# Optimization experiments

Hardware: AMD Instinct MI355X
Metric: run time of the kernel (lower is better)

Reference implementation:

```python
import jax, jax.numpy as jnp
import numpy as np

N_NODES = 10000
N_EDGES = 320000
MUL0, MUL1 = 64, 32        # input irreps: 64x0e + 32x1e
EDGE_DIM = 64
W_NUMEL = 224              # 64+64+32+32+32 per-edge uvu path weights
DENOM = 32.0
SQRT3 = 3.0 ** 0.5
INV_SQRT3 = 1.0 / SQRT3
INV_SQRT2 = 2.0 ** -0.5


def setup_inputs() -> dict:
    key = jax.random.key(0)
    ks = jax.random.split(key, 12)

    def lin(k, fi, fo):
        return (jax.random.normal(k, (fi, fo), jnp.float32) / np.float32(np.sqrt(fi)))

    return {
        "node_feature": jax.random.normal(ks[0], (N_NODES, MUL0 + 3 * MUL1), jnp.float32),
        "edge_attr": jax.random.normal(ks[1], (N_EDGES, 3), jnp.float32),
        "edge_feature": jax.random.normal(ks[2], (N_EDGES, EDGE_DIM), jnp.float32),
        "W_skip0": lin(ks[3], MUL0, 96),
        "W_skip1": lin(ks[4], MUL1, 32),
        "W_nl0": lin(ks[5], MUL0, MUL0),
        "W_nl1": lin(ks[6], MUL1, MUL1),
        "W_fc1": lin(ks[7], EDGE_DIM, 64),
        "W_fc2": lin(ks[8], 64, W_NUMEL),
        "W_out_s": lin(ks[9], 96, 96),
        "W_out_v": lin(ks[10], 128, 32),
        "edge_index": jax.random.randint(ks[11], (2, N_EDGES), 0, N_NODES),
    }


def _forward(node_feature, edge_attr, edge_feature, W_skip0, W_skip1, W_nl0, W_nl1,
             W_fc1, W_fc2, W_out_s, W_out_v, edge_index):
    N = node_feature.shape[0]
    E = edge_attr.shape[0]
    s = node_feature[:, :MUL0]                       # [N,64] l=0 scalars
    v = node_feature[:, MUL0:].reshape(N, MUL1, 3)   # [N,32,3] l=1 vectors

    # skip_linear: in_irreps -> gate irreps (96x0e + 32x1e); per-l mixing of multiplicities
    skip_s = s @ W_skip0
    skip_v = jnp.einsum('nmi,mk->nki', v, W_skip1)

    # node_linear: in_irreps -> in_irreps
    s = s @ W_nl0
    v = jnp.einsum('nmi,mk->nki', v, W_nl1)

    # spherical harmonics (normalize=True, 'component'): Y0 = 1, Y1 = sqrt(3) * r_hat
    rhat = edge_attr / jnp.linalg.norm(edge_attr, axis=-1, keepdims=True)
    sh1 = SQRT3 * rhat                               # [E,3]

    # edge-conditioned TP weights: FC net (relu MLP, no bias)
    w = jax.nn.relu(edge_feature @ W_fc1) @ W_fc2    # [E,224]
    w0, w1, w2, w3, w4 = jnp.split(w, [64, 128, 160, 192], axis=-1)

    src, dst = edge_index[0], edge_index[1]
    xs = s[dst]                                      # gather: [E,64]
    xv = v[dst]                                      # gather: [E,32,3]

    # uvu CG paths (sh0 component == 1)
    out0a = w0 * xs                                                         # 0e x 0e -> 0e
    out0b = w3 * (jnp.einsum('emi,ei->em', xv, sh1) * INV_SQRT3)            # 1e x 1e -> 0e
    out1a = (w1 * xs)[:, :, None] * sh1[:, None, :]                         # 0e x 1e -> 1e
    out1b = w2[:, :, None] * xv                                             # 1e x 0e -> 1e
    out1c = w4[:, :, None] * (jnp.cross(xv, sh1[:, None, :]) * INV_SQRT2)   # 1e x 1e -> 1e

    # sorted irreps_mid layout: [96 scalars | 128 vectors * 3] = 480
    tp = jnp.concatenate([out0a, out0b,
                          out1a.reshape(E, -1), out1b.reshape(E, -1), out1c.reshape(E, -1)],
                         axis=-1)                    # [E,480]

    # scatter-sum to destination nodes, then divide by denominator
    agg = jax.ops.segment_sum(tp, src, num_segments=N) / DENOM

    # dropout(p=0.0) on l=0 channels -> identity
    agg_s = agg[:, :96]
    agg_v = agg[:, 96:].reshape(N, 128, 3)

    # node_linear_2: tp_irreps_out -> gate irreps, plus skip connection
    out_s = agg_s @ W_out_s + skip_s
    out_v = jnp.einsum('nmi,mk->nki', agg_v, W_out_v) + skip_v

    # equivariant gate: 64 scalars (silu) | 32 gate scalars (sigmoid) * 32 vectors
    fs = jax.nn.silu(out_s[:, :MUL0])
    gate = jax.nn.sigmoid(out_s[:, MUL0:MUL0 + 32])
    gv = gate[:, :, None] * out_v
    return jnp.concatenate([fs, gv.reshape(N, -1)], axis=-1)  # [N,160]


def reference(node_feature, edge_attr, edge_feature, W_skip0, W_skip1, W_nl0, W_nl1,
              W_fc1, W_fc2, W_out_s, W_out_v, edge_index):
    return _forward(node_feature, edge_attr, edge_feature, W_skip0, W_skip1, W_nl0, W_nl1,
                    W_fc1, W_fc2, W_out_s, W_out_v, edge_index)
```

## Files before the change

kernel.cpp:

```cpp
#include <hip/hip_runtime.h>
#include <math.h>

#define N_NODES 10000
#define N_EDGES 320000
#define TILES 8
#define NBLK (N_EDGES / (32 * TILES))

#define SQRT3F     1.7320508075688772f
#define INV_SQRT3F 0.5773502691896258f
#define INV_SQRT2F 0.7071067811865476f

typedef short bf16x8 __attribute__((ext_vector_type(8)));
typedef short b16x4  __attribute__((ext_vector_type(4)));
typedef float f32x4  __attribute__((ext_vector_type(4)));
typedef unsigned int u32;

static __device__ __forceinline__ unsigned short f2b(float f) {
    unsigned int u = __float_as_uint(f);
    unsigned int r = (u + 0x7fffu + ((u >> 16) & 1u)) >> 16;
    return (unsigned short)r;
}
static __device__ __forceinline__ float b2f(unsigned short h) {
    return __uint_as_float(((unsigned int)h) << 16);
}

static __device__ __forceinline__ void gl_lds16(const void* g, void* l) {
    __builtin_amdgcn_global_load_lds(
        (const __attribute__((address_space(1))) u32*)g,
        (__attribute__((address_space(3))) u32*)l,
        16, 0, 0);
}

__global__ __launch_bounds__(256) void prep_kernel(
    const float* __restrict__ nf,
    const float* __restrict__ Wnl0,
    const float* __restrict__ Wnl1,
    const float* __restrict__ Wfc1,
    const float* __restrict__ Wfc2,
    const float* __restrict__ Wout_s,
    const float* __restrict__ Wout_v,
    const float* __restrict__ Wskip0,
    const float* __restrict__ Wskip1,
    const int* __restrict__ eidx,
    float* __restrict__ st_vt32,
    unsigned short* __restrict__ st_vt16,
    unsigned short* __restrict__ W1T,
    unsigned short* __restrict__ W2T,
    unsigned short* __restrict__ WsCombT,
    unsigned short* __restrict__ WvCombT,
    int* __restrict__ cnt)
{
    const int b = blockIdx.x;
    const int tid = threadIdx.x;
    if (b < 6250) {
        int gid = b * 256 + tid;
        if (gid >= N_NODES * 160) return;
        int n = gid / 160;
        int j = gid - n * 160;
        const float* nfn = nf + (size_t)n * 160;
        float acc = 0.f;
        if (j < 64) {
            #pragma unroll 8
            for (int k = 0; k < 64; ++k) acc += nfn[k] * Wnl0[k * 64 + j];
        } else {
            int t = j - 64;
            int i = t >> 5, k = t & 31;
            #pragma unroll 8
            for (int m = 0; m < 32; ++m) acc += nfn[64 + m * 3 + i] * Wnl1[m * 32 + k];
        }
        st_vt32[(size_t)n * 160 + j] = acc;
        st_vt16[(size_t)n * 160 + j] = f2b(acc);
    } else if (b < 7500) {
        int e = (b - 6250) * 256 + tid;
        if (e < N_EDGES) atomicAdd(&cnt[eidx[e]], 1);
    } else if (b < 7572) {
        int idx = (b - 7500) * 256 + tid;
        if (idx < 4096) {
            int n = idx >> 6, k = idx & 63;
            W1T[idx] = f2b(Wfc1[k * 64 + n]);
        } else if (idx < 18432) {
            int j = idx - 4096;
            int n = j >> 6, k = j & 63;
            W2T[j] = f2b(Wfc2[k * 224 + n]);
        }
    } else {
        int idx = (b - 7572) * 256 + tid;
        if (idx < 15360) {
            int n = idx / 160, k = idx - n * 160;
            float v = (k < 96) ? Wout_s[k * 96 + n] : Wskip0[(k - 96) * 96 + n];
            WsCombT[idx] = f2b(v);
        } else if (idx < 20480) {
            int j = idx - 15360;
            int n = j / 160, k = j - n * 160;
            float v = (k < 128) ? Wout_v[k * 32 + n] : Wskip1[(k - 128) * 32 + n];
            WvCombT[j] = f2b(v);
        }
    }
}

__global__ __launch_bounds__(1024) void scan_kernel(
    const int* __restrict__ cnt, int* __restrict__ row_start)
{
    __shared__ int part[1024];
    const int t = threadIdx.x;
    const int CH = 10;
    int base = t * CH;
    int s = 0;
    for (int i = 0; i < CH; ++i) {
        int idx = base + i;
        if (idx < N_NODES) s += cnt[idx];
    }
    part[t] = s;
    __syncthreads();
    for (int off = 1; off < 1024; off <<= 1) {
        int v = (t >= off) ? part[t - off] : 0;
        __syncthreads();
        part[t] += v;
        __syncthreads();
    }
    int run = (t == 0) ? 0 : part[t - 1];
    for (int i = 0; i < CH; ++i) {
        int idx = base + i;
        if (idx < N_NODES) { row_start[idx] = run; run += cnt[idx]; }
    }
    if (t == 1023) row_start[N_NODES] = run;
}

__global__ __launch_bounds__(256) void scatter_kernel(
    const int* __restrict__ eidx, const float* __restrict__ edge_attr,
    const int* __restrict__ row_start,
    int* __restrict__ fill, int* __restrict__ order,
    int* __restrict__ src_srt, int* __restrict__ dst_srt,
    float* __restrict__ sh_srt)
{
    int e = blockIdx.x * 256 + threadIdx.x;
    if (e >= N_EDGES) return;
    int s = eidx[e];
    int p = atomicAdd(&fill[s], 1) + row_start[s];
    order[p] = e;
    src_srt[p] = s;
    dst_srt[p] = eidx[N_EDGES + e];
    float x = edge_attr[(size_t)e * 3 + 0];
    float y = edge_attr[(size_t)e * 3 + 1];
    float z = edge_attr[(size_t)e * 3 + 2];
    float inv = SQRT3F / sqrtf(x * x + y * y + z * z);
    sh_srt[(size_t)p * 4 + 0] = x * inv;
    sh_srt[(size_t)p * 4 + 1] = y * inv;
    sh_srt[(size_t)p * 4 + 2] = z * inv;
    sh_srt[(size_t)p * 4 + 3] = 0.f;
}

__global__ __launch_bounds__(256, 7) void edge_mlp(
    const unsigned short* __restrict__ W1T,
    const unsigned short* __restrict__ W2T,
    const int* __restrict__ order,
    const float* __restrict__ edge_feature,
    unsigned short* __restrict__ w_srt)
{
    __shared__ __align__(16) unsigned short A1[32 * 64];
    __shared__ __align__(16) unsigned short Hs[32 * 64];
    __shared__ __align__(16) unsigned short w_s[32 * 224];
    __shared__ int eid_s[32 * TILES];

    const int tid  = threadIdx.x;
    const int lane = tid & 63;
    const int wv   = tid >> 6;
    const int l15  = lane & 15;
    const int g    = lane >> 4;
    const int p0   = blockIdx.x * (32 * TILES);

    bf16x8 w1b0 = *reinterpret_cast<const bf16x8*>(&W1T[(wv * 16 + l15) * 64 + g * 8]);
    bf16x8 w1b1 = *reinterpret_cast<const bf16x8*>(&W1T[(wv * 16 + l15) * 64 + 32 + g * 8]);
    bf16x8 w2b0[4], w2b1[4];
    #pragma unroll
    for (int ii = 0; ii < 4; ++ii) {
        int nt = wv * 4 + ii;
        w2b0[ii] = *reinterpret_cast<const bf16x8*>(&W2T[(nt * 16 + l15) * 64 + g * 8]);
        w2b1[ii] = *reinterpret_cast<const bf16x8*>(&W2T[(nt * 16 + l15) * 64 + 32 + g * 8]);
    }

    if (tid < 32 * TILES) eid_s[tid] = order[p0 + tid];
    __syncthreads();

    f32x4 efr[2];
    auto load_ef = [&](int t) {
        int ebase = t * 32;
        #pragma unroll
        for (int r = 0; r < 2; ++r) {
            int q = tid + r * 256;
            int el = q >> 4, qf = q & 15;
            efr[r] = *reinterpret_cast<const f32x4*>(
                edge_feature + (size_t)eid_s[ebase + el] * 64 + qf * 4);
        }
    };
    auto write_ef = [&]() {
        #pragma unroll
        for (int r = 0; r < 2; ++r) {
            int q = tid + r * 256;
            int el = q >> 4, f0 = (q & 15) * 4;
            b16x4 h;
            #pragma unroll
            for (int j = 0; j < 4; ++j) h[j] = (short)f2b(efr[r][j]);
            *reinterpret_cast<b16x4*>(&A1[el * 64 + (f0 ^ ((el & 7) << 3))]) = h;
        }
    };

    load_ef(0);

    for (int t = 0; t < TILES; ++t) {
        write_ef();
        __syncthreads();
        if (t < TILES - 1) load_ef(t + 1);

        {
            const int nt = wv;
            #pragma unroll
            for (int mt = 0; mt < 2; ++mt) {
                f32x4 c4 = {0.f, 0.f, 0.f, 0.f};
                int ra = mt * 16 + l15;
                int sw = (ra & 7) << 3;
                bf16x8 a0 = *reinterpret_cast<const bf16x8*>(&A1[ra * 64 + ((g * 8) ^ sw)]);
                bf16x8 a1 = *reinterpret_cast<const bf16x8*>(&A1[ra * 64 + ((32 + g * 8) ^ sw)]);
                c4 = __builtin_amdgcn_mfma_f32_16x16x32_bf16(a0, w1b0, c4, 0, 0, 0);
                c4 = __builtin_amdgcn_mfma_f32_16x16x32_bf16(a1, w1b1, c4, 0, 0, 0);
                #pragma unroll
                for (int r = 0; r < 4; ++r) {
                    int row = mt * 16 + g * 4 + r;
                    int col = nt * 16 + l15;
                    Hs[row * 64 + (col ^ ((row & 7) << 3))] = f2b(fmaxf(c4[r], 0.f));
                }
            }
        }
        __syncthreads();

        {
            #pragma unroll
            for (int ii = 0; ii < 4; ++ii) {
                int nt = wv * 4 + ii;
                #pragma unroll
                for (int mt = 0; mt < 2; ++mt) {
                    f32x4 c4 = {0.f, 0.f, 0.f, 0.f};
                    int ra = mt * 16 + l15;
                    int sw = (ra & 7) << 3;
                    bf16x8 a0 = *reinterpret_cast<const bf16x8*>(&Hs[ra * 64 + ((g * 8) ^ sw)]);
                    bf16x8 a1 = *reinterpret_cast<const bf16x8*>(&Hs[ra * 64 + ((32 + g * 8) ^ sw)]);
                    c4 = __builtin_amdgcn_mfma_f32_16x16x32_bf16(a0, w2b0[ii], c4, 0, 0, 0);
                    c4 = __builtin_amdgcn_mfma_f32_16x16x32_bf16(a1, w2b1[ii], c4, 0, 0, 0);
                    if (nt < 14) {
                        #pragma unroll
                        for (int r = 0; r < 4; ++r) {
                            int row = mt * 16 + g * 4 + r;
                            w_s[row * 224 + nt * 16 + l15] = f2b(c4[r]);
                        }
                    }
                }
            }
        }
        __syncthreads();

        {
            const size_t gbase = (size_t)(p0 + t * 32) * 224;
            for (int idx = tid; idx < 896; idx += 256) {
                *reinterpret_cast<f32x4*>(&w_srt[gbase + idx * 8]) =
                    *reinterpret_cast<const f32x4*>(&w_s[idx * 8]);
            }
        }
    }
}

__global__ __launch_bounds__(256, 7) void node_msg(
    const int* __restrict__ row_start,
    const int* __restrict__ dst_srt,
    const float* __restrict__ sh_srt,
    const unsigned short* __restrict__ w_srt,
    const float* __restrict__ st_vt32,
    float* __restrict__ agg)
{
    __shared__ __align__(16) float df[32 * 160];
    __shared__ float aggbuf[480];
    __shared__ float sh_c[32][4];

    const int n   = (blockIdx.x & 7) * 1250 + (blockIdx.x >> 3);
    const int tid = threadIdx.x;
    const int p_start = row_start[n];
    const int p_end   = row_start[n + 1];

    const int tid2 = tid & 127;
    const int half = tid >> 7;
    int region, cb, iv;
    if (tid2 < 48)       { region = 0; cb = tid2 & 15;        iv = tid2 >> 4; }
    else if (tid2 < 64)  { region = 1; cb = tid2 - 48;        iv = 0; }
    else if (tid2 < 88)  { region = 2; cb = (tid2 - 64) & 7;  iv = (tid2 - 64) >> 3; }
    else if (tid2 < 112) { region = 3; cb = (tid2 - 88) & 7;  iv = (tid2 - 88) >> 3; }
    else if (tid2 < 120) { region = 4; cb = tid2 - 112;       iv = 0; }
    else                 { region = 5; cb = 0; iv = 0; }
    int rbase = 0, woff = 0, doff = 0;
    if (region == 0)      { rbase = 96 + iv * 64 + 4 * cb;  woff = 64 + 4 * cb;  doff = 4 * cb; }
    else if (region == 1) { rbase = 4 * cb;                 woff = 4 * cb;       doff = 4 * cb; }
    else if (region == 2) { rbase = 288 + iv * 32 + 4 * cb; woff = 128 + 4 * cb; doff = 64 + iv * 32 + 4 * cb; }
    else if (region == 3) { rbase = 384 + iv * 32 + 4 * cb; woff = 192 + 4 * cb; }
    else if (region == 4) { rbase = 64 + 4 * cb;            woff = 160 + 4 * cb; }
    int i1 = iv + 1; if (i1 == 3) i1 = 0;
    int i2 = 3 - iv - i1;

    f32x4 acc = {0.f, 0.f, 0.f, 0.f};

    for (int pb = p_start; pb < p_end; pb += 32) {
        const int nvalid = min(p_end - pb, 32);
        const int qlimit = nvalid * 40;
        __syncthreads();

        if (tid < nvalid) {
            *reinterpret_cast<f32x4*>(&sh_c[tid][0]) =
                *reinterpret_cast<const f32x4*>(&sh_srt[(size_t)(pb + tid) * 4]);
        }
        #pragma unroll
        for (int r = 0; r < 5; ++r) {
            int idx = tid + r * 256;
            if (idx < qlimit) {
                int el = idx / 40, off = idx - el * 40;
                int d = dst_srt[pb + el];
                gl_lds16(st_vt32 + (size_t)d * 160 + off * 4, &df[idx * 4]);
            }
        }
        __syncthreads();

        if (region < 5) {
            const int e0l = half * 16;
            #pragma unroll 4
            for (int j2 = 0; j2 < 16; ++j2) {
                int el = e0l + j2;
                if (el >= nvalid) break;
                const float* dfp = &df[el * 160];
                const unsigned short* we = w_srt + (size_t)(pb + el) * 224;
                b16x4 w = *reinterpret_cast<const b16x4*>(we + woff);
                if (region == 0) {
                    f32x4 x = *reinterpret_cast<const f32x4*>(dfp + doff);
                    float sh = sh_c[el][iv];
                    #pragma unroll
                    for (int j = 0; j < 4; ++j)
                        acc[j] += b2f((unsigned short)w[j]) * x[j] * sh;
                } else if (region == 1 || region == 2) {
                    f32x4 x = *reinterpret_cast<const f32x4*>(dfp + doff);
                    #pragma unroll
                    for (int j = 0; j < 4; ++j)
                        acc[j] += b2f((unsigned short)w[j]) * x[j];
                } else if (region == 3) {
                    f32x4 xA = *reinterpret_cast<const f32x4*>(dfp + 64 + i1 * 32 + 4 * cb);
                    f32x4 xB = *reinterpret_cast<const f32x4*>(dfp + 64 + i2 * 32 + 4 * cb);
                    float shA = sh_c[el][i1], shB = sh_c[el][i2];
                    #pragma unroll
                    for (int j = 0; j < 4; ++j)
                        acc[j] += b2f((unsigned short)w[j]) *
                                  (xA[j] * shB - xB[j] * shA) * INV_SQRT2F;
                } else {
                    f32x4 x0 = *reinterpret_cast<const f32x4*>(dfp + 64 + 4 * cb);
                    f32x4 x1 = *reinterpret_cast<const f32x4*>(dfp + 96 + 4 * cb);
                    f32x4 x2 = *reinterpret_cast<const f32x4*>(dfp + 128 + 4 * cb);
                    float s0 = sh_c[el][0], s1 = sh_c[el][1], s2 = sh_c[el][2];
                    #pragma unroll
                    for (int j = 0; j < 4; ++j)
                        acc[j] += b2f((unsigned short)w[j]) *
                                  (x0[j] * s0 + x1[j] * s1 + x2[j] * s2) * INV_SQRT3F;
                }
            }
        }
    }

    __syncthreads();
    if (half == 0 && region < 5) {
        #pragma unroll
        for (int j = 0; j < 4; ++j) aggbuf[rbase + j] = acc[j];
    }
    __syncthreads();
    if (half == 1 && region < 5) {
        #pragma unroll
        for (int j = 0; j < 4; ++j) aggbuf[rbase + j] += acc[j];
    }
    __syncthreads();
    if (tid < 120) {
        *reinterpret_cast<f32x4*>(&agg[(size_t)n * 480 + tid * 4]) =
            *reinterpret_cast<const f32x4*>(&aggbuf[tid * 4]);
    }
}

__global__ __launch_bounds__(256) void out_gemm(
    const float* __restrict__ agg,
    const float* __restrict__ nf,
    const unsigned short* __restrict__ WsCombT,
    const unsigned short* __restrict__ WvCombT,
    float* __restrict__ out)
{
    __shared__ float os_l[32][96];
    __shared__ float ov_l[3][32][32];

    const int n0  = blockIdx.x * 32;
    const int tid = threadIdx.x;
    const int lane = tid & 63;
    const int wv   = tid >> 6;
    const int l15  = lane & 15;
    const int g    = lane >> 4;

    #pragma unroll
    for (int jj = 0; jj < 6; ++jj) {
        int job = wv * 6 + jj;
        bool isS;
        int mt, nt, ii = 0;
        if (job < 12) { isS = true;  mt = job & 1; nt = job >> 1; }
        else { int j = job - 12; isS = false; ii = j >> 2; mt = (j >> 1) & 1; nt = j & 1; }

        int ra = mt * 16 + l15;
        int n  = min(n0 + ra, N_NODES - 1);
        const float* aggn = agg + (size_t)n * 480;
        const float* nfn  = nf + (size_t)n * 160;
        const unsigned short* WT = isS ? WsCombT : WvCombT;

        f32x4 c4 = {0.f, 0.f, 0.f, 0.f};
        #pragma unroll
        for (int kk = 0; kk < 5; ++kk) {
            int k0 = kk * 32 + g * 8;
            float av[8];
            if (isS) {
                if (k0 < 96) {
                    f32x4 p0 = *reinterpret_cast<const f32x4*>(aggn + k0);
                    f32x4 p1 = *reinterpret_cast<const f32x4*>(aggn + k0 + 4);
                    #pragma unroll
                    for (int j = 0; j < 4; ++j) { av[j] = p0[j] * (1.f/32.f); av[4+j] = p1[j] * (1.f/32.f); }
                } else {
                    f32x4 p0 = *reinterpret_cast<const f32x4*>(nfn + (k0 - 96));
                    f32x4 p1 = *reinterpret_cast<const f32x4*>(nfn + (k0 - 96) + 4);
                    #pragma unroll
                    for (int j = 0; j < 4; ++j) { av[j] = p0[j]; av[4+j] = p1[j]; }
                }
            } else {
                if (k0 < 128) {
                    int base = (k0 < 64) ? (96 + ii * 64 + k0)
                             : (k0 < 96) ? (288 + ii * 32 + (k0 - 64))
                                         : (384 + ii * 32 + (k0 - 96));
                    f32x4 p0 = *reinterpret_cast<const f32x4*>(aggn + base);
                    f32x4 p1 = *reinterpret_cast<const f32x4*>(aggn + base + 4);
                    #pragma unroll
                    for (int j = 0; j < 4; ++j) { av[j] = p0[j] * (1.f/32.f); av[4+j] = p1[j] * (1.f/32.f); }
                } else {
                    #pragma unroll
                    for (int j = 0; j < 8; ++j)
                        av[j] = nfn[64 + (k0 - 128 + j) * 3 + ii];
                }
            }
            bf16x8 a;
            #pragma unroll
            for (int j = 0; j < 8; ++j) a[j] = (short)f2b(av[j]);
            bf16x8 bfr = *reinterpret_cast<const bf16x8*>(
                WT + (size_t)(nt * 16 + l15) * 160 + k0);
            c4 = __builtin_amdgcn_mfma_f32_16x16x32_bf16(a, bfr, c4, 0, 0, 0);
        }
        #pragma unroll
        for (int r = 0; r < 4; ++r) {
            int row = mt * 16 + g * 4 + r;
            int col = nt * 16 + l15;
            if (isS) os_l[row][col] = c4[r];
            else     ov_l[ii][row][col] = c4[r];
        }
    }
    __syncthreads();

    for (int idx = tid; idx < 32 * 160; idx += 256) {
        int r = idx / 160, c = idx - r * 160;
        int n = n0 + r;
        if (n < N_NODES) {
            if (c < 64) {
                float x = os_l[r][c];
                out[(size_t)n * 160 + c] = x / (1.f + expf(-x));
            } else {
                int t = c - 64;
                int k = t / 3, i = t - 3 * k;
                float gg = os_l[r][64 + k];
                gg = 1.f / (1.f + expf(-gg));
                out[(size_t)n * 160 + c] = gg * ov_l[i][r][k];
            }
        }
    }
}

__global__ __launch_bounds__(256, 3) void edge_conv_fused(
    const unsigned short* __restrict__ W1T,
    const unsigned short* __restrict__ W2T,
    const int* __restrict__ order,
    const int* __restrict__ src_srt,
    const int* __restrict__ dst_srt,
    const float* __restrict__ sh_srt,
    const float* __restrict__ edge_feature,
    const unsigned short* __restrict__ st_vt16,
    float* __restrict__ agg)
{
    __shared__ __align__(16) unsigned short A1[32 * 64];
    __shared__ __align__(16) unsigned short Hs[32 * 64];
    __shared__ __align__(16) unsigned short w_s[32 * 224];
    __shared__ __align__(16) unsigned short df[2][32 * 160];
    __shared__ int   eid_s[32 * TILES];
    __shared__ int   src_s[32 * TILES];
    __shared__ int   dst_s[32 * TILES];
    __shared__ float sh_s[32 * TILES][4];

    const int tid  = threadIdx.x;
    const int lane = tid & 63;
    const int wv   = tid >> 6;
    const int l15  = lane & 15;
    const int g    = lane >> 4;
    const int p0   = blockIdx.x * (32 * TILES);

    bf16x8 w1b0 = *reinterpret_cast<const bf16x8*>(&W1T[(wv * 16 + l15) * 64 + g * 8]);
    bf16x8 w1b1 = *reinterpret_cast<const bf16x8*>(&W1T[(wv * 16 + l15) * 64 + 32 + g * 8]);
    bf16x8 w2b0[4], w2b1[4];
    #pragma unroll
    for (int ii = 0; ii < 4; ++ii) {
        int nt = wv * 4 + ii;
        w2b0[ii] = *reinterpret_cast<const bf16x8*>(&W2T[(nt * 16 + l15) * 64 + g * 8]);
        w2b1[ii] = *reinterpret_cast<const bf16x8*>(&W2T[(nt * 16 + l15) * 64 + 32 + g * 8]);
    }

    for (int b = tid; b < 32 * TILES; b += 256) {
        int p = p0 + b;
        eid_s[b] = order[p];
        src_s[b] = src_srt[p];
        dst_s[b] = dst_srt[p];
        *reinterpret_cast<f32x4*>(&sh_s[b][0]) =
            *reinterpret_cast<const f32x4*>(&sh_srt[(size_t)p * 4]);
    }
    __syncthreads();

    const int tid2 = tid & 127;
    int region, cb, iv;
    if (tid2 < 48)       { region = 0; cb = tid2 & 15;        iv = tid2 >> 4; }
    else if (tid2 < 64)  { region = 1; cb = tid2 - 48;        iv = 0; }
    else if (tid2 < 88)  { region = 2; cb = (tid2 - 64) & 7;  iv = (tid2 - 64) >> 3; }
    else if (tid2 < 112) { region = 3; cb = (tid2 - 88) & 7;  iv = (tid2 - 88) >> 3; }
    else if (tid2 < 120) { region = 4; cb = tid2 - 112;       iv = 0; }
    else                 { region = 5; cb = 0; iv = 0; }
    int rbase = 0, woff = 0, doff = 0;
    if (region == 0)      { rbase = 96 + iv * 64 + 4 * cb;  woff = 64 + 4 * cb;  doff = 4 * cb; }
    else if (region == 1) { rbase = 4 * cb;                 woff = 4 * cb;       doff = 4 * cb; }
    else if (region == 2) { rbase = 288 + iv * 32 + 4 * cb; woff = 128 + 4 * cb; doff = 64 + iv * 32 + 4 * cb; }
    else if (region == 3) { rbase = 384 + iv * 32 + 4 * cb; woff = 192 + 4 * cb; }
    else if (region == 4) { rbase = 64 + 4 * cb;            woff = 160 + 4 * cb; }
    int i1 = iv + 1; if (i1 == 3) i1 = 0;
    int i2 = 3 - iv - i1;

    f32x4 acc = {0.f, 0.f, 0.f, 0.f};
    int cur = src_s[(tid >> 7) * 16];

    f32x4 efr[2];
    auto load_ef = [&](int t) {
        int ebase = t * 32;
        #pragma unroll
        for (int r = 0; r < 2; ++r) {
            int q = tid + r * 256;
            int el = q >> 4, qf = q & 15;
            efr[r] = *reinterpret_cast<const f32x4*>(
                edge_feature + (size_t)eid_s[ebase + el] * 64 + qf * 4);
        }
    };
    auto write_ef = [&]() {
        #pragma unroll
        for (int r = 0; r < 2; ++r) {
            int q = tid + r * 256;
            int el = q >> 4, f0 = (q & 15) * 4;
            b16x4 h;
            #pragma unroll
            for (int j = 0; j < 4; ++j) h[j] = (short)f2b(efr[r][j]);
            *reinterpret_cast<b16x4*>(&A1[el * 64 + (f0 ^ ((el & 7) << 3))]) = h;
        }
    };
    auto issue_df = [&](int t, int b) {
        int ebase = t * 32;
        #pragma unroll
        for (int r = 0; r < 3; ++r) {
            int idx = tid + r * 256;
            if (idx < 640) {
                int el = idx / 20, off = idx - el * 20;
                gl_lds16(st_vt16 + (size_t)dst_s[ebase + el] * 160 + off * 8,
                         &df[b][idx * 8]);
            }
        }
    };

    issue_df(0, 0);
    load_ef(0);

    for (int t = 0; t < TILES; ++t) {
        const int b = t & 1;
        write_ef();
        __syncthreads();
        if (t < TILES - 1) {
            issue_df(t + 1, b ^ 1);
            load_ef(t + 1);
        }
        {
            const int nt = wv;
            #pragma unroll
            for (int mt = 0; mt < 2; ++mt) {
                f32x4 c4 = {0.f, 0.f, 0.f, 0.f};
                int ra = mt * 16 + l15;
                int sw = (ra & 7) << 3;
                bf16x8 a0 = *reinterpret_cast<const bf16x8*>(&A1[ra * 64 + ((g * 8) ^ sw)]);
                bf16x8 a1 = *reinterpret_cast<const bf16x8*>(&A1[ra * 64 + ((32 + g * 8) ^ sw)]);
                c4 = __builtin_amdgcn_mfma_f32_16x16x32_bf16(a0, w1b0, c4, 0, 0, 0);
                c4 = __builtin_amdgcn_mfma_f32_16x16x32_bf16(a1, w1b1, c4, 0, 0, 0);
                #pragma unroll
                for (int r = 0; r < 4; ++r) {
                    int row = mt * 16 + g * 4 + r;
                    int col = nt * 16 + l15;
                    Hs[row * 64 + (col ^ ((row & 7) << 3))] = f2b(fmaxf(c4[r], 0.f));
                }
            }
        }
        __syncthreads();
        {
            #pragma unroll
            for (int ii = 0; ii < 4; ++ii) {
                int nt = wv * 4 + ii;
                #pragma unroll
                for (int mt = 0; mt < 2; ++mt) {
                    f32x4 c4 = {0.f, 0.f, 0.f, 0.f};
                    int ra = mt * 16 + l15;
                    int sw = (ra & 7) << 3;
                    bf16x8 a0 = *reinterpret_cast<const bf16x8*>(&Hs[ra * 64 + ((g * 8) ^ sw)]);
                    bf16x8 a1 = *reinterpret_cast<const bf16x8*>(&Hs[ra * 64 + ((32 + g * 8) ^ sw)]);
                    c4 = __builtin_amdgcn_mfma_f32_16x16x32_bf16(a0, w2b0[ii], c4, 0, 0, 0);
                    c4 = __builtin_amdgcn_mfma_f32_16x16x32_bf16(a1, w2b1[ii], c4, 0, 0, 0);
                    if (nt < 14) {
                        #pragma unroll
                        for (int r = 0; r < 4; ++r) {
                            int row = mt * 16 + g * 4 + r;
                            w_s[row * 224 + nt * 16 + l15] = f2b(c4[r]);
                        }
                    }
                }
            }
        }
        __syncthreads();
        if (region < 5) {
            const int e0l = (tid >> 7) * 16;
            #pragma unroll 4
            for (int j2 = 0; j2 < 16; ++j2) {
                int el = e0l + j2;
                int eg = t * 32 + el;
                int s = src_s[eg];
                if (s != cur) {
                    #pragma unroll
                    for (int j = 0; j < 4; ++j)
                        atomicAdd(&agg[(size_t)cur * 480 + rbase + j], acc[j]);
                    acc = (f32x4){0.f, 0.f, 0.f, 0.f};
                    cur = s;
                }
                const unsigned short* dfp = &df[b][el * 160];
                const unsigned short* we  = &w_s[el * 224];
                b16x4 w = *reinterpret_cast<const b16x4*>(we + woff);
                if (region == 0) {
                    b16x4 x = *reinterpret_cast<const b16x4*>(dfp + doff);
                    float sh = sh_s[eg][iv];
                    #pragma unroll
                    for (int j = 0; j < 4; ++j)
                        acc[j] += b2f((unsigned short)w[j]) * b2f((unsigned short)x[j]) * sh;
                } else if (region == 1 || region == 2) {
                    b16x4 x = *reinterpret_cast<const b16x4*>(dfp + doff);
                    #pragma unroll
                    for (int j = 0; j < 4; ++j)
                        acc[j] += b2f((unsigned short)w[j]) * b2f((unsigned short)x[j]);
                } else if (region == 3) {
                    b16x4 xA = *reinterpret_cast<const b16x4*>(dfp + 64 + i1 * 32 + 4 * cb);
                    b16x4 xB = *reinterpret_cast<const b16x4*>(dfp + 64 + i2 * 32 + 4 * cb);
                    float shA = sh_s[eg][i1], shB = sh_s[eg][i2];
                    #pragma unroll
                    for (int j = 0; j < 4; ++j)
                        acc[j] += b2f((unsigned short)w[j]) *
                                  (b2f((unsigned short)xA[j]) * shB -
                                   b2f((unsigned short)xB[j]) * shA) * INV_SQRT2F;
                } else {
                    b16x4 x0 = *reinterpret_cast<const b16x4*>(dfp + 64 + 4 * cb);
                    b16x4 x1 = *reinterpret_cast<const b16x4*>(dfp + 96 + 4 * cb);
                    b16x4 x2 = *reinterpret_cast<const b16x4*>(dfp + 128 + 4 * cb);
                    float s0 = sh_s[eg][0], s1 = sh_s[eg][1], s2 = sh_s[eg][2];
                    #pragma unroll
                    for (int j = 0; j < 4; ++j)
                        acc[j] += b2f((unsigned short)w[j]) *
                                  (b2f((unsigned short)x0[j]) * s0 +
                                   b2f((unsigned short)x1[j]) * s1 +
                                   b2f((unsigned short)x2[j]) * s2) * INV_SQRT3F;
                }
            }
        }
    }
    if (region < 5) {
        #pragma unroll
        for (int j = 0; j < 4; ++j)
            atomicAdd(&agg[(size_t)cur * 480 + rbase + j], acc[j]);
    }
}

__global__ __launch_bounds__(128) void out_kernel(
    const float* __restrict__ agg,
    const float* __restrict__ nf,
    const float* __restrict__ Wskip0,
    const float* __restrict__ Wskip1,
    const float* __restrict__ Wout_s,
    const float* __restrict__ Wout_v,
    float* __restrict__ out)
{
    __shared__ float aggl[480];
    __shared__ float os_s[96];
    const int n = blockIdx.x;
    const int tid = threadIdx.x;
    const float* nfn = nf + (size_t)n * 160;

    for (int idx = tid; idx < 480; idx += 128)
        aggl[idx] = agg[(size_t)n * 480 + idx] * (1.f / 32.f);
    __syncthreads();

    if (tid < 96) {
        float acc = 0.f;
        #pragma unroll 8
        for (int k = 0; k < 64; ++k) acc += nfn[k] * Wskip0[k * 96 + tid];
        for (int r = 0; r < 96; ++r) acc += aggl[r] * Wout_s[r * 96 + tid];
        os_s[tid] = acc;
    }
    __syncthreads();

    if (tid < 64) {
        float x = os_s[tid];
        out[(size_t)n * 160 + tid] = x / (1.f + expf(-x));
    }
    if (tid < 96) {
        int t = tid;
        int k = t / 3, i = t - 3 * k;
        float acc = 0.f;
        #pragma unroll 8
        for (int m = 0; m < 32; ++m) acc += nfn[64 + m * 3 + i] * Wskip1[m * 32 + k];
        #pragma unroll 8
        for (int m = 0; m < 64; ++m) acc += aggl[96 + i * 64 + m] * Wout_v[m * 32 + k];
        #pragma unroll 8
        for (int m = 0; m < 32; ++m) acc += aggl[288 + i * 32 + m] * Wout_v[(64 + m) * 32 + k];
        #pragma unroll 8
        for (int m = 0; m < 32; ++m) acc += aggl[384 + i * 32 + m] * Wout_v[(96 + m) * 32 + k];
        float g = os_s[64 + k];
        g = 1.f / (1.f + expf(-g));
        out[(size_t)n * 160 + 64 + t] = g * acc;
    }
}

extern "C" void kernel_launch(void* const* d_in, const int* in_sizes, int n_in,
                              void* d_out, int out_size, void* d_ws, size_t ws_size,
                              hipStream_t stream)
{
    const float* nf     = (const float*)d_in[0];
    const float* ea     = (const float*)d_in[1];
    const float* ef     = (const float*)d_in[2];
    const float* Wskip0 = (const float*)d_in[3];
    const float* Wskip1 = (const float*)d_in[4];
    const float* Wnl0   = (const float*)d_in[5];
    const float* Wnl1   = (const float*)d_in[6];
    const float* Wfc1   = (const float*)d_in[7];
    const float* Wfc2   = (const float*)d_in[8];
    const float* Wout_s = (const float*)d_in[9];
    const float* Wout_v = (const float*)d_in[10];
    const int*   eidx   = (const int*)d_in[11];
    float* out = (float*)d_out;

    int*   cnt       = (int*)d_ws;
    int*   fill      = cnt + 10000;
    int*   row_start = fill + 10000;
    int*   order     = row_start + 10004;
    int*   src_srt   = order + 320000;
    int*   dst_srt   = src_srt + 320000;
    float* sh_srt    = (float*)(dst_srt + 320000);
    float* agg       = sh_srt + 1280000;
    float* st_vt32   = agg + 4800000;
    unsigned short* st_vt16 = (unsigned short*)(st_vt32 + 1600000);
    unsigned short* W1T     = st_vt16 + 1600000;
    unsigned short* W2T     = W1T + 4096;
    unsigned short* WsCombT = W2T + 16384;
    unsigned short* WvCombT = WsCombT + 15360;
    unsigned short* w_srt   = WvCombT + 5152;

    const size_t need_split =
        (size_t)((const char*)(w_srt + (size_t)(N_EDGES + 32) * 224) - (const char*)d_ws);
    const bool use_split = (ws_size >= need_split);

    hipMemsetAsync(cnt, 0, 20000 * sizeof(int), stream);

    prep_kernel<<<7652, 256, 0, stream>>>(
        nf, Wnl0, Wnl1, Wfc1, Wfc2, Wout_s, Wout_v, Wskip0, Wskip1,
        eidx, st_vt32, st_vt16, W1T, W2T, WsCombT, WvCombT, cnt);

    scan_kernel<<<1, 1024, 0, stream>>>(cnt, row_start);
    scatter_kernel<<<(N_EDGES + 255) / 256, 256, 0, stream>>>(
        eidx, ea, row_start, fill, order, src_srt, dst_srt, sh_srt);

    if (use_split) {
        edge_mlp<<<NBLK, 256, 0, stream>>>(W1T, W2T, order, ef, w_srt);
        node_msg<<<N_NODES, 256, 0, stream>>>(
            row_start, dst_srt, sh_srt, w_srt, st_vt32, agg);
        out_gemm<<<(N_NODES + 31) / 32, 256, 0, stream>>>(
            agg, nf, WsCombT, WvCombT, out);
    } else {
        hipMemsetAsync(agg, 0, (size_t)N_NODES * 480 * sizeof(float), stream);
        edge_conv_fused<<<NBLK, 256, 0, stream>>>(
            W1T, W2T, order, src_srt, dst_srt, sh_srt, ef, st_vt16, agg);
        out_kernel<<<N_NODES, 128, 0, stream>>>(
            agg, nf, Wskip0, Wskip1, Wout_s, Wout_v, out);
    }
}
```

Before: 270.7 us.

## Double-buffer node_msg over 8-node groups and move node linear to MFMA

```diff
diff --git a/kernel.cpp b/kernel.cpp
--- a/kernel.cpp
+++ b/kernel.cpp
@@ -31,10 +31,88 @@
         16, 0, 0);
 }
 
-__global__ __launch_bounds__(256) void prep_kernel(
+__global__ __launch_bounds__(256) void nt_mfma(
     const float* __restrict__ nf,
     const float* __restrict__ Wnl0,
     const float* __restrict__ Wnl1,
+    float* __restrict__ st_vt32,
+    unsigned short* __restrict__ st_vt16)
+{
+    __shared__ __align__(16) float nf_l[32 * 160];
+
+    const int n0  = blockIdx.x * 32;
+    const int tid = threadIdx.x;
+    const int lane = tid & 63;
+    const int wv   = tid >> 6;
+    const int l15  = lane & 15;
+    const int g    = lane >> 4;
+
+    #pragma unroll
+    for (int r = 0; r < 5; ++r) {
+        int idx = tid + r * 256;
+        int row = idx / 40, off = idx - row * 40;
+        int n = min(n0 + row, N_NODES - 1);
+        *reinterpret_cast<f32x4*>(&nf_l[row * 160 + off * 4]) =
+            *reinterpret_cast<const f32x4*>(nf + (size_t)n * 160 + off * 4);
+    }
+    __syncthreads();
+
+    #pragma unroll
+    for (int jj = 0; jj < 5; ++jj) {
+        int job = wv * 5 + jj;
+        f32x4 c4 = {0.f, 0.f, 0.f, 0.f};
+        int colbase;
+        if (job < 8) {
+            int mt = job & 1, nt = job >> 1;
+            int row = mt * 16 + l15;
+            #pragma unroll
+            for (int kk = 0; kk < 2; ++kk) {
+                int k0 = kk * 32 + g * 8;
+                bf16x8 a, b;
+                #pragma unroll
+                for (int j = 0; j < 8; ++j) {
+                    a[j] = (short)f2b(nf_l[row * 160 + k0 + j]);
+                    b[j] = (short)f2b(Wnl0[(k0 + j) * 64 + nt * 16 + l15]);
+                }
+                c4 = __builtin_amdgcn_mfma_f32_16x16x32_bf16(a, b, c4, 0, 0, 0);
+            }
+            colbase = nt * 16 + l15;
+            #pragma unroll
+            for (int r = 0; r < 4; ++r) {
+                int rr = mt * 16 + g * 4 + r;
+                int n = n0 + rr;
+                if (n < N_NODES) {
+                    st_vt32[(size_t)n * 160 + colbase] = c4[r];
+                    st_vt16[(size_t)n * 160 + colbase] = f2b(c4[r]);
+                }
+            }
+        } else {
+            int j2 = job - 8;
+            int i = j2 >> 2, nt = (j2 >> 1) & 1, mt = j2 & 1;
+            int row = mt * 16 + l15;
+            bf16x8 a, b;
+            #pragma unroll
+            for (int j = 0; j < 8; ++j) {
+                int k = g * 8 + j;
+                a[j] = (short)f2b(nf_l[row * 160 + 64 + k * 3 + i]);
+                b[j] = (short)f2b(Wnl1[k * 32 + nt * 16 + l15]);
+            }
+            c4 = __builtin_amdgcn_mfma_f32_16x16x32_bf16(a, b, c4, 0, 0, 0);
+            colbase = 64 + i * 32 + nt * 16 + l15;
+            #pragma unroll
+            for (int r = 0; r < 4; ++r) {
+                int rr = mt * 16 + g * 4 + r;
+                int n = n0 + rr;
+                if (n < N_NODES) {
+                    st_vt32[(size_t)n * 160 + colbase] = c4[r];
+                    st_vt16[(size_t)n * 160 + colbase] = f2b(c4[r]);
+                }
+            }
+        }
+    }
+}
+
+__global__ __launch_bounds__(256) void prep_kernel(
     const float* __restrict__ Wfc1,
     const float* __restrict__ Wfc2,
     const float* __restrict__ Wout_s,
@@ -42,8 +120,6 @@
     const float* __restrict__ Wskip0,
     const float* __restrict__ Wskip1,
     const int* __restrict__ eidx,
-    float* __restrict__ st_vt32,
-    unsigned short* __restrict__ st_vt16,
     unsigned short* __restrict__ W1T,
     unsigned short* __restrict__ W2T,
     unsigned short* __restrict__ WsCombT,
@@ -52,29 +128,11 @@
 {
     const int b = blockIdx.x;
     const int tid = threadIdx.x;
-    if (b < 6250) {
-        int gid = b * 256 + tid;
-        if (gid >= N_NODES * 160) return;
-        int n = gid / 160;
-        int j = gid - n * 160;
-        const float* nfn = nf + (size_t)n * 160;
-        float acc = 0.f;
-        if (j < 64) {
-            #pragma unroll 8
-            for (int k = 0; k < 64; ++k) acc += nfn[k] * Wnl0[k * 64 + j];
-        } else {
-            int t = j - 64;
-            int i = t >> 5, k = t & 31;
-            #pragma unroll 8
-            for (int m = 0; m < 32; ++m) acc += nfn[64 + m * 3 + i] * Wnl1[m * 32 + k];
-        }
-        st_vt32[(size_t)n * 160 + j] = acc;
-        st_vt16[(size_t)n * 160 + j] = f2b(acc);
-    } else if (b < 7500) {
-        int e = (b - 6250) * 256 + tid;
+    if (b < 1250) {
+        int e = b * 256 + tid;
         if (e < N_EDGES) atomicAdd(&cnt[eidx[e]], 1);
-    } else if (b < 7572) {
-        int idx = (b - 7500) * 256 + tid;
+    } else if (b < 1322) {
+        int idx = (b - 1250) * 256 + tid;
         if (idx < 4096) {
             int n = idx >> 6, k = idx & 63;
             W1T[idx] = f2b(Wfc1[k * 64 + n]);
@@ -84,7 +142,7 @@
             W2T[j] = f2b(Wfc2[k * 224 + n]);
         }
     } else {
-        int idx = (b - 7572) * 256 + tid;
+        int idx = (b - 1322) * 256 + tid;
         if (idx < 15360) {
             int n = idx / 160, k = idx - n * 160;
             float v = (k < 96) ? Wout_s[k * 96 + n] : Wskip0[(k - 96) * 96 + n];
@@ -268,7 +326,7 @@
     }
 }
 
-__global__ __launch_bounds__(256, 7) void node_msg(
+__global__ __launch_bounds__(256, 2) void node_msg(
     const int* __restrict__ row_start,
     const int* __restrict__ dst_srt,
     const float* __restrict__ sh_srt,
@@ -276,14 +334,19 @@
     const float* __restrict__ st_vt32,
     float* __restrict__ agg)
 {
-    __shared__ __align__(16) float df[32 * 160];
+    __shared__ __align__(16) float df[2][32 * 160];
+    __shared__ __align__(16) unsigned short w_l[2][32 * 224];
+    __shared__ float sh_c[2][32][4];
     __shared__ float aggbuf[480];
-    __shared__ float sh_c[32][4];
-
-    const int n   = (blockIdx.x & 7) * 1250 + (blockIdx.x >> 3);
+    __shared__ int   psh[9];
+
     const int tid = threadIdx.x;
-    const int p_start = row_start[n];
-    const int p_end   = row_start[n + 1];
+    const int xcd = blockIdx.x & 7, bi = blockIdx.x >> 3;
+    const int grp = (xcd < 2) ? xcd * 157 + bi : 2 * 157 + (xcd - 2) * 156 + bi;
+    const int nb  = grp * 8;
+
+    if (tid < 9) psh[tid] = row_start[nb + tid];
+    __syncthreads();
 
     const int tid2 = tid & 127;
     const int half = tid >> 7;
@@ -303,84 +366,110 @@
     int i1 = iv + 1; if (i1 == 3) i1 = 0;
     int i2 = 3 - iv - i1;
 
-    f32x4 acc = {0.f, 0.f, 0.f, 0.f};
-
-    for (int pb = p_start; pb < p_end; pb += 32) {
-        const int nvalid = min(p_end - pb, 32);
-        const int qlimit = nvalid * 40;
-        __syncthreads();
-
-        if (tid < nvalid) {
-            *reinterpret_cast<f32x4*>(&sh_c[tid][0]) =
-                *reinterpret_cast<const f32x4*>(&sh_srt[(size_t)(pb + tid) * 4]);
+    auto stage = [&](int pb, int b) {
+        if (tid < 32) {
+            int pp = min(pb + tid, N_EDGES - 1);
+            *reinterpret_cast<f32x4*>(&sh_c[b][tid][0]) =
+                *reinterpret_cast<const f32x4*>(&sh_srt[(size_t)pp * 4]);
         }
         #pragma unroll
         for (int r = 0; r < 5; ++r) {
             int idx = tid + r * 256;
-            if (idx < qlimit) {
-                int el = idx / 40, off = idx - el * 40;
-                int d = dst_srt[pb + el];
-                gl_lds16(st_vt32 + (size_t)d * 160 + off * 4, &df[idx * 4]);
-            }
-        }
-        __syncthreads();
-
-        if (region < 5) {
-            const int e0l = half * 16;
-            #pragma unroll 4
-            for (int j2 = 0; j2 < 16; ++j2) {
-                int el = e0l + j2;
-                if (el >= nvalid) break;
-                const float* dfp = &df[el * 160];
-                const unsigned short* we = w_srt + (size_t)(pb + el) * 224;
-                b16x4 w = *reinterpret_cast<const b16x4*>(we + woff);
-                if (region == 0) {
-                    f32x4 x = *reinterpret_cast<const f32x4*>(dfp + doff);
-                    float sh = sh_c[el][iv];
-                    #pragma unroll
-                    for (int j = 0; j < 4; ++j)
-                        acc[j] += b2f((unsigned short)w[j]) * x[j] * sh;
-                } else if (region == 1 || region == 2) {
-                    f32x4 x = *reinterpret_cast<const f32x4*>(dfp + doff);
-                    #pragma unroll
-                    for (int j = 0; j < 4; ++j)
-                        acc[j] += b2f((unsigned short)w[j]) * x[j];
-                } else if (region == 3) {
-                    f32x4 xA = *reinterpret_cast<const f32x4*>(dfp + 64 + i1 * 32 + 4 * cb);
-                    f32x4 xB = *reinterpret_cast<const f32x4*>(dfp + 64 + i2 * 32 + 4 * cb);
-                    float shA = sh_c[el][i1], shB = sh_c[el][i2];
-                    #pragma unroll
-                    for (int j = 0; j < 4; ++j)
-                        acc[j] += b2f((unsigned short)w[j]) *
-                                  (xA[j] * shB - xB[j] * shA) * INV_SQRT2F;
-                } else {
-                    f32x4 x0 = *reinterpret_cast<const f32x4*>(dfp + 64 + 4 * cb);
-                    f32x4 x1 = *reinterpret_cast<const f32x4*>(dfp + 96 + 4 * cb);
-                    f32x4 x2 = *reinterpret_cast<const f32x4*>(dfp + 128 + 4 * cb);
-                    float s0 = sh_c[el][0], s1 = sh_c[el][1], s2 = sh_c[el][2];
-                    #pragma unroll
-                    for (int j = 0; j < 4; ++j)
-                        acc[j] += b2f((unsigned short)w[j]) *
-                                  (x0[j] * s0 + x1[j] * s1 + x2[j] * s2) * INV_SQRT3F;
-                }
-            }
-        }
-    }
-
+            int el = idx / 40, off = idx - el * 40;
+            int pp = min(pb + el, N_EDGES - 1);
+            gl_lds16(st_vt32 + (size_t)dst_srt[pp] * 160 + off * 4,
+                     &df[b][idx * 4]);
+        }
+        #pragma unroll
+        for (int r = 0; r < 4; ++r) {
+            int idx = tid + r * 256;
+            if (idx < 896) {
+                gl_lds16(w_srt + (size_t)pb * 224 + idx * 8, &w_l[b][idx * 8]);
+            }
+        }
+    };
+
+    f32x4 acc = {0.f, 0.f, 0.f, 0.f};
+
+    int fg = 0;
+    while (fg < 8 && psh[fg] >= psh[fg + 1]) ++fg;
+    if (fg < 8) stage(psh[fg], 0);
     __syncthreads();
-    if (half == 0 && region < 5) {
-        #pragma unroll
-        for (int j = 0; j < 4; ++j) aggbuf[rbase + j] = acc[j];
-    }
-    __syncthreads();
-    if (half == 1 && region < 5) {
-        #pragma unroll
-        for (int j = 0; j < 4; ++j) aggbuf[rbase + j] += acc[j];
-    }
-    __syncthreads();
-    if (tid < 120) {
-        *reinterpret_cast<f32x4*>(&agg[(size_t)n * 480 + tid * 4]) =
-            *reinterpret_cast<const f32x4*>(&aggbuf[tid * 4]);
+    int buf = 0;
+
+    for (int g2 = 0; g2 < 8; ++g2) {
+        const int pe = psh[g2 + 1];
+        for (int pb = psh[g2]; pb < pe; pb += 32) {
+            {
+                int ng = g2, npb = pb + 32;
+                if (npb >= pe) {
+                    ng = g2 + 1;
+                    while (ng < 8 && psh[ng] >= psh[ng + 1]) ++ng;
+                    npb = (ng < 8) ? psh[ng] : 0;
+                }
+                if (ng < 8) stage(npb, buf ^ 1);
+            }
+            const int nvalid = min(pe - pb, 32);
+            if (region < 5) {
+                const int e0l = half * 16;
+                #pragma unroll 4
+                for (int j2 = 0; j2 < 16; ++j2) {
+                    int el = e0l + j2;
+                    if (el >= nvalid) break;
+                    const float* dfp = &df[buf][el * 160];
+                    const unsigned short* we = &w_l[buf][el * 224];
+                    b16x4 w = *reinterpret_cast<const b16x4*>(we + woff);
+                    if (region == 0) {
+                        f32x4 x = *reinterpret_cast<const f32x4*>(dfp + doff);
+                        float sh = sh_c[buf][el][iv];
+                        #pragma unroll
+                        for (int j = 0; j < 4; ++j)
+                            acc[j] += b2f((unsigned short)w[j]) * x[j] * sh;
+                    } else if (region == 1 || region == 2) {
+                        f32x4 x = *reinterpret_cast<const f32x4*>(dfp + doff);
+                        #pragma unroll
+                        for (int j = 0; j < 4; ++j)
+                            acc[j] += b2f((unsigned short)w[j]) * x[j];
+                    } else if (region == 3) {
+                        f32x4 xA = *reinterpret_cast<const f32x4*>(dfp + 64 + i1 * 32 + 4 * cb);
+                        f32x4 xB = *reinterpret_cast<const f32x4*>(dfp + 64 + i2 * 32 + 4 * cb);
+                        float shA = sh_c[buf][el][i1], shB = sh_c[buf][el][i2];
+                        #pragma unroll
+                        for (int j = 0; j < 4; ++j)
+                            acc[j] += b2f((unsigned short)w[j]) *
+                                      (xA[j] * shB - xB[j] * shA) * INV_SQRT2F;
+                    } else {
+                        f32x4 x0 = *reinterpret_cast<const f32x4*>(dfp + 64 + 4 * cb);
+                        f32x4 x1 = *reinterpret_cast<const f32x4*>(dfp + 96 + 4 * cb);
+                        f32x4 x2 = *reinterpret_cast<const f32x4*>(dfp + 128 + 4 * cb);
+                        float s0 = sh_c[buf][el][0], s1 = sh_c[buf][el][1], s2 = sh_c[buf][el][2];
+                        #pragma unroll
+                        for (int j = 0; j < 4; ++j)
+                            acc[j] += b2f((unsigned short)w[j]) *
+                                      (x0[j] * s0 + x1[j] * s1 + x2[j] * s2) * INV_SQRT3F;
+                    }
+                }
+            }
+            __syncthreads();
+            buf ^= 1;
+        }
+
+        if (half == 0 && region < 5) {
+            #pragma unroll
+            for (int j = 0; j < 4; ++j) aggbuf[rbase + j] = acc[j];
+        }
+        __syncthreads();
+        if (half == 1 && region < 5) {
+            #pragma unroll
+            for (int j = 0; j < 4; ++j) aggbuf[rbase + j] += acc[j];
+        }
+        __syncthreads();
+        if (tid < 120) {
+            *reinterpret_cast<f32x4*>(&agg[(size_t)(nb + g2) * 480 + tid * 4]) =
+                *reinterpret_cast<const f32x4*>(&aggbuf[tid * 4]);
+        }
+        acc = (f32x4){0.f, 0.f, 0.f, 0.f};
+        __syncthreads();
     }
 }
 
@@ -788,9 +877,12 @@
 
     hipMemsetAsync(cnt, 0, 20000 * sizeof(int), stream);
 
-    prep_kernel<<<7652, 256, 0, stream>>>(
-        nf, Wnl0, Wnl1, Wfc1, Wfc2, Wout_s, Wout_v, Wskip0, Wskip1,
-        eidx, st_vt32, st_vt16, W1T, W2T, WsCombT, WvCombT, cnt);
+    nt_mfma<<<(N_NODES + 31) / 32, 256, 0, stream>>>(
+        nf, Wnl0, Wnl1, st_vt32, st_vt16);
+
+    prep_kernel<<<1402, 256, 0, stream>>>(
+        Wfc1, Wfc2, Wout_s, Wout_v, Wskip0, Wskip1,
+        eidx, W1T, W2T, WsCombT, WvCombT, cnt);
 
     scan_kernel<<<1, 1024, 0, stream>>>(cnt, row_start);
     scatter_kernel<<<(N_EDGES + 255) / 256, 256, 0, stream>>>(
@@ -798,7 +890,7 @@
 
     if (use_split) {
         edge_mlp<<<NBLK, 256, 0, stream>>>(W1T, W2T, order, ef, w_srt);
-        node_msg<<<N_NODES, 256, 0, stream>>>(
+        node_msg<<<1250, 256, 0, stream>>>(
             row_start, dst_srt, sh_srt, w_srt, st_vt32, agg);
         out_gemm<<<(N_NODES + 31) / 32, 256, 0, stream>>>(
             agg, nf, WsCombT, WvCombT, out);
```

Result: slower. 346.3 us (+27.9%).
